# Performance work log

Hardware: AMD Instinct MI355X
Metric: run time of the kernel (lower is better)

The kernel has to match this reference:

```python
import jax, jax.numpy as jnp
import numpy as np

B, E, FC_N = 8, 65536, 2500
CONVS = [5, 16, 32, 64, 64]
EPS = 1e-5


def setup_inputs() -> dict:
    key = jax.random.key(0)
    ks = iter(jax.random.split(key, 32))
    inp = {
        'x': jax.random.normal(next(ks), (B, 5, E), dtype=jnp.float32),
        'gemm': jax.random.randint(next(ks), (B, E, 4), 0, E, dtype=jnp.int32),
        'old_verts': jax.random.normal(next(ks), (B, 642, 3), dtype=jnp.float32),
    }
    for i in range(4):
        ci, co = CONVS[i], CONVS[i + 1]
        inp[f'w{i}'] = jax.random.normal(next(ks), (co, ci, 5), dtype=jnp.float32) * 0.02
        inp[f'b{i}'] = jnp.zeros((co,), dtype=jnp.float32)
        inp[f'g{i}'] = jnp.ones((co,), dtype=jnp.float32)
        inp[f'beta{i}'] = jnp.zeros((co,), dtype=jnp.float32)
    inp['dw1'] = jax.random.normal(next(ks), (FC_N, CONVS[-1]), dtype=jnp.float32) * 0.02
    inp['db1'] = jnp.zeros((FC_N,), dtype=jnp.float32)
    inp['dw2'] = jax.random.normal(next(ks), (642 * 3, FC_N), dtype=jnp.float32) * 0.02
    inp['db2'] = jnp.zeros((642 * 3,), dtype=jnp.float32)
    return inp


def mesh_conv(x, gemm, w, b):
    # x: (B,C,E); gemm: (B,E,4) -> neighbor features (B,C,E,4)
    nb = jax.vmap(lambda xb, gb: xb[:, gb])(x, gemm)
    # MeshCNN symmetric features: [self, a+c, b+d, |a-c|, |b-d|]
    f = jnp.stack([
        x,
        nb[..., 0] + nb[..., 2],
        nb[..., 1] + nb[..., 3],
        jnp.abs(nb[..., 0] - nb[..., 2]),
        jnp.abs(nb[..., 1] - nb[..., 3]),
    ], axis=-1)  # (B,C,E,5)
    return jnp.einsum('bcek,ock->boe', f, w) + b[None, :, None]


def bn_relu(x, g, beta):
    # BatchNorm2d training-mode math over (batch, spatial) per channel
    mean = jnp.mean(x, axis=(0, 2), keepdims=True)
    var = jnp.var(x, axis=(0, 2), keepdims=True)
    return jax.nn.relu((x - mean) * jax.lax.rsqrt(var + EPS) * g[None, :, None] + beta[None, :, None])


def reference(x, gemm, old_verts,
              w0, b0, g0, beta0, w1, b1, g1, beta1,
              w2, b2, g2, beta2, w3, b3, g3, beta3,
              dw1, db1, dw2, db2):
    h = x[:, :5]
    params = [(w0, b0, g0, beta0), (w1, b1, g1, beta1),
              (w2, b2, g2, beta2), (w3, b3, g3, beta3)]
    for w, b, g, beta in params:
        h = bn_relu(mesh_conv(h, gemm, w, b), g, beta)
    pooled = jnp.mean(h, axis=2)                 # AvgPool1d(n_edges) -> (B, C)
    h1 = jax.nn.relu(pooled @ dw1.T + db1)       # dropout = identity (eval)
    out = h1 @ dw2.T + db2
    return out.reshape(-1, 642, 3) + old_verts
```

## Files before the change

kernel.cpp:

```cpp
#include <hip/hip_runtime.h>

#define E_DIM 65536
#define BE_TOTAL 524288
#define EPS_BN 1e-5f
#define NB_STATS 256

typedef unsigned int uint;
typedef unsigned short ushort;
typedef unsigned char uchar;
typedef __attribute__((ext_vector_type(4))) float floatx4;

#define PB_FP8 ((size_t)BE_TOTAL*16)

__device__ __forceinline__ float bflo(uint u){ return __uint_as_float(u << 16); }
__device__ __forceinline__ float bfhi(uint u){ return __uint_as_float(u & 0xffff0000u); }

__device__ __forceinline__ ushort pbf1(float a){
  uint ua = __float_as_uint(a);
  return (ushort)((ua + 0x7fffu + ((ua >> 16) & 1u)) >> 16);
}
__device__ __forceinline__ uint packbf(float a, float b){
  return (uint)pbf1(a) | ((uint)pbf1(b) << 16);
}
__device__ __forceinline__ void unpack8(uint4 v, float* x){
  x[0]=bflo(v.x); x[1]=bfhi(v.x); x[2]=bflo(v.y); x[3]=bfhi(v.y);
  x[4]=bflo(v.z); x[5]=bfhi(v.z); x[6]=bflo(v.w); x[7]=bfhi(v.w);
}

__device__ __forceinline__ uint2 pack8f8(const float* z){
  int lo = __builtin_amdgcn_cvt_pk_fp8_f32(z[0], z[1], 0,  false);
  lo     = __builtin_amdgcn_cvt_pk_fp8_f32(z[2], z[3], lo, true);
  int hi = __builtin_amdgcn_cvt_pk_fp8_f32(z[4], z[5], 0,  false);
  hi     = __builtin_amdgcn_cvt_pk_fp8_f32(z[6], z[7], hi, true);
  uint2 r; r.x = (uint)lo; r.y = (uint)hi; return r;
}
__device__ __forceinline__ void dec8f8(uint2 w, float* x){
  x[0]=__builtin_amdgcn_cvt_f32_fp8((int)w.x,0);
  x[1]=__builtin_amdgcn_cvt_f32_fp8((int)w.x,1);
  x[2]=__builtin_amdgcn_cvt_f32_fp8((int)w.x,2);
  x[3]=__builtin_amdgcn_cvt_f32_fp8((int)w.x,3);
  x[4]=__builtin_amdgcn_cvt_f32_fp8((int)w.y,0);
  x[5]=__builtin_amdgcn_cvt_f32_fp8((int)w.y,1);
  x[6]=__builtin_amdgcn_cvt_f32_fp8((int)w.y,2);
  x[7]=__builtin_amdgcn_cvt_f32_fp8((int)w.y,3);
}
__device__ __forceinline__ uchar f8byte(float v){
  return (uchar)(__builtin_amdgcn_cvt_pk_fp8_f32(v, 0.f, 0, false) & 0xff);
}

template<int CI, int CO>
__global__ void wprep8(const float* __restrict__ w, uchar* __restrict__ img)
{
  constexpr int CHUNKS = CI/16;
  const int t = blockIdx.x*256 + threadIdx.x;
  if (t >= CHUNKS*3*CO*4) return;
  const int g  = t & 3;
  const int o  = (t >> 2) % CO;
  const int ck = (t >> 2) / CO;
  const int chunk = ck / 3;
  const int ks    = ck % 3;
  float z[8];
  #pragma unroll
  for (int j8=0;j8<8;j8++){
    const int j = g*8 + j8;
    const int ft = ks*2 + (j>>4);
    const int ci = chunk*16 + (j & 15);
    z[j8] = (ft < 5) ? w[((size_t)o*CI + ci)*5 + ft] * 64.f : 0.f;
  }
  const int t4 = (o&3) ^ ((o>>2)&3);
  *reinterpret_cast<uint2*>(img + ((size_t)(ck*CO + o))*32 + ((g^t4)<<3)) = pack8f8(z);
}

template<int CI, int CO>
__launch_bounds__(512, 1)
__global__ void mconv_mfma(const char* __restrict__ hin,
                           const int* __restrict__ gemm,
                           const char* __restrict__ wimg,
                           const float* __restrict__ bias, float bscale,
                           const float* __restrict__ ss, float pkf,
                           char* __restrict__ hout,
                           float* __restrict__ spart)
{
  constexpr int CHUNKS = CI/16;
  constexpr int NT = CO/16;
  constexpr int FBY = 3*256*32;
  constexpr int NBUF = (CHUNKS > 1) ? 2 : 1;
  constexpr int OBB = 256*CO;
  constexpr int SBY = 8*2*CO*4;
  constexpr int SMEM = (NBUF*FBY > OBB+SBY) ? NBUF*FBY : (OBB+SBY);
  __shared__ char smem[SMEM];
  char* FB = smem;

  const int tid = threadIdx.x;
  const int bid = blockIdx.x;
  const int b   = bid & 7;
  const int e0  = (bid >> 3) * 256;
  const size_t bbase = (size_t)b << 16;

  const int lane = tid & 63;
  const int wv   = tid >> 6;
  const int col  = lane & 15;
  const int kg   = lane >> 4;
  const int t4c  = (col & 3) ^ ((col >> 2) & 3);

  floatx4 acc[2][NT];
  #pragma unroll
  for (int n=0;n<NT;n++){
    const float bv = bias[n*16 + col] * bscale;
    #pragma unroll
    for (int mt=0;mt<2;mt++) acc[mt][n] = (floatx4){bv,bv,bv,bv};
  }

  const int el = tid >> 1;
  const int hh = tid & 1;
  const int t4e = (el&3) ^ ((el>>2)&3);
  uint off[5];
  {
    const size_t idx = bbase + (size_t)(e0 + el);
    const int4 g4 = *reinterpret_cast<const int4*>(gemm + idx*4);
    off[0] = (uint)(idx*16 + hh*8);
    off[1] = (uint)((bbase + (size_t)(uint)g4.x)*16 + hh*8);
    off[2] = (uint)((bbase + (size_t)(uint)g4.y)*16 + hh*8);
    off[3] = (uint)((bbase + (size_t)(uint)g4.z)*16 + hh*8);
    off[4] = (uint)((bbase + (size_t)(uint)g4.w)*16 + hh*8);
  }

  auto BUILD = [&](uint2 (&q)[5], int chunk, char* FBb){
    float v[5][8];
    #pragma unroll
    for (int r=0;r<5;r++) dec8f8(q[r], v[r]);
    const int cb = chunk*16 + hh*8;
    #pragma unroll
    for (int c=0;c<8;c++){
      const float sc = ss[cb+c], sh = ss[CI+cb+c];
      #pragma unroll
      for (int r=0;r<5;r++) v[r][c] = fmaxf(fmaf(v[r][c], sc, sh), 0.f);
    }
    float y[5][8];
    #pragma unroll
    for (int c=0;c<8;c++){
      y[0][c] = v[0][c];
      y[1][c] = v[1][c] + v[3][c];
      y[2][c] = v[2][c] + v[4][c];
      y[3][c] = fabsf(v[1][c] - v[3][c]);
      y[4][c] = fabsf(v[2][c] - v[4][c]);
    }
    #pragma unroll
    for (int ks=0; ks<3; ks++){
      char* base = FBb + ks*8192 + el*32;
      *reinterpret_cast<uint2*>(base + (((0+hh)^t4e)<<3)) = pack8f8(y[2*ks]);
      if (ks < 2){
        *reinterpret_cast<uint2*>(base + (((2+hh)^t4e)<<3)) = pack8f8(y[2*ks+1]);
      } else {
        uint2 zz; zz.x=0u; zz.y=0u;
        *reinterpret_cast<uint2*>(base + (((2+hh)^t4e)<<3)) = zz;
      }
    }
  };

  auto MMA = [&](int chunk, const char* FBb){
    const char* WG = wimg + (size_t)chunk*(3*CO*32);
    #pragma unroll
    for (int ks=0; ks<3; ks++){
      long long bf[NT];
      #pragma unroll
      for (int n=0;n<NT;n++)
        bf[n] = *reinterpret_cast<const long long*>(WG + ks*(CO*32) + n*512 + col*32 + ((kg^t4c)<<3));
      #pragma unroll
      for (int mt=0;mt<2;mt++){
        const long long af = *reinterpret_cast<const long long*>(
            FBb + ks*8192 + (wv*32+mt*16+col)*32 + ((kg^t4c)<<3));
        #pragma unroll
        for (int n=0;n<NT;n++)
          acc[mt][n] = __builtin_amdgcn_mfma_f32_16x16x32_fp8_fp8(af, bf[n], acc[mt][n], 0, 0, 0);
      }
    }
  };

  if constexpr (CHUNKS == 1){
    uint2 q[5];
    #pragma unroll
    for (int r=0;r<5;r++) q[r] = *reinterpret_cast<const uint2*>(hin + off[r]);
    BUILD(q, 0, FB);
    __syncthreads();
    MMA(0, FB);
  } else {
    uint2 qs[2][5];
    #pragma unroll
    for (int r=0;r<5;r++) qs[0][r] = *reinterpret_cast<const uint2*>(hin + off[r]);
    {
      const char* hp1 = hin + PB_FP8;
      #pragma unroll
      for (int r=0;r<5;r++) qs[1][r] = *reinterpret_cast<const uint2*>(hp1 + off[r]);
    }
    BUILD(qs[0], 0, FB);
    __syncthreads();
    #pragma unroll
    for (int c=0; c<CHUNKS; ++c){
      if (c+2 < CHUNKS){
        const char* hp = hin + (size_t)(c+2)*PB_FP8;
        #pragma unroll
        for (int r=0;r<5;r++) qs[c&1][r] = *reinterpret_cast<const uint2*>(hp + off[r]);
      }
      MMA(c, FB + (c&1)*FBY);
      if (c+1 < CHUNKS){
        BUILD(qs[(c+1)&1], c+1, FB + ((c+1)&1)*FBY);
        __syncthreads();
      }
    }
  }

  float sred[2*NT];
  #pragma unroll
  for (int n=0;n<NT;n++){
    float s = 0.f, q2 = 0.f;
    #pragma unroll
    for (int mt=0;mt<2;mt++){
      #pragma unroll
      for (int r=0;r<4;r++){ const float vv = acc[mt][n][r]; s += vv; q2 = fmaf(vv,vv,q2); }
    }
    s  += __shfl_xor(s,16,64);  s  += __shfl_xor(s,32,64);
    q2 += __shfl_xor(q2,16,64); q2 += __shfl_xor(q2,32,64);
    sred[n] = s; sred[NT+n] = q2;
  }

  __syncthreads();
  float* SB = reinterpret_cast<float*>(smem + OBB);
  {
    uchar* OB = reinterpret_cast<uchar*>(smem);
    #pragma unroll
    for (int mt=0; mt<2; mt++){
      const int er = wv*32 + mt*16 + 4*kg;
      #pragma unroll
      for (int n=0;n<NT;n++){
        #pragma unroll
        for (int r=0;r<4;r++)
          OB[(er+r)*CO + n*16 + col] = f8byte(acc[mt][n][r] * pkf);
      }
    }
  }
  if (kg == 0){
    #pragma unroll
    for (int n=0;n<NT;n++){
      SB[wv*2*CO + n*16 + col]      = sred[n];
      SB[wv*2*CO + CO + n*16 + col] = sred[NT+n];
    }
  }
  __syncthreads();
  {
    constexpr int NV = 256*CO/16;
    for (int i=tid; i<NV; i+=512){
      const int pl  = i >> 8;
      const int elx = i & 255;
      const uint4 vv = *reinterpret_cast<const uint4*>(smem + elx*CO + pl*16);
      *reinterpret_cast<uint4*>(hout + (size_t)pl*PB_FP8 + (bbase + (size_t)(e0+elx))*16) = vv;
    }
  }
  if (tid < 2*CO){
    float s = 0.f;
    #pragma unroll
    for (int w8=0; w8<8; w8++) s += SB[w8*2*CO + tid];
    spart[(size_t)bid*2*CO + tid] = s;
  }
}

__launch_bounds__(256)
__global__ void conv0_kernel(const ushort* __restrict__ hin,
                             const int* __restrict__ gemm,
                             const float* __restrict__ w,
                             const float* __restrict__ bias,
                             char* __restrict__ hout)
{
  const int bid = blockIdx.x;
  const int swz = (bid & 7) * 256 + (bid >> 3);
  const int idx = swz * 256 + threadIdx.x;
  const int b = idx >> 16;
  const int4 g4 = *reinterpret_cast<const int4*>(gemm + (size_t)idx * 4);
  const size_t bbase = (size_t)b << 16;
  float xc[8], n0[8], n1[8], n2[8], n3[8];
  unpack8(*reinterpret_cast<const uint4*>(hin + (size_t)idx*8), xc);
  unpack8(*reinterpret_cast<const uint4*>(hin + (bbase + (size_t)(uint)g4.x)*8), n0);
  unpack8(*reinterpret_cast<const uint4*>(hin + (bbase + (size_t)(uint)g4.y)*8), n1);
  unpack8(*reinterpret_cast<const uint4*>(hin + (bbase + (size_t)(uint)g4.z)*8), n2);
  unpack8(*reinterpret_cast<const uint4*>(hin + (bbase + (size_t)(uint)g4.w)*8), n3);
  float f1[5], f2[5], f3[5], f4[5];
  #pragma unroll
  for (int c=0;c<5;c++){
    f1[c] = n0[c] + n2[c];
    f2[c] = n1[c] + n3[c];
    f3[c] = fabsf(n0[c] - n2[c]);
    f4[c] = fabsf(n1[c] - n3[c]);
  }
  float acc[16];
  #pragma unroll
  for (int o=0;o<16;o++){
    const float* wp = w + (size_t)o*25;
    float a = bias[o];
    #pragma unroll
    for (int c=0;c<5;c++){
      a = fmaf(xc[c], wp[c*5+0], a);
      a = fmaf(f1[c], wp[c*5+1], a);
      a = fmaf(f2[c], wp[c*5+2], a);
      a = fmaf(f3[c], wp[c*5+3], a);
      a = fmaf(f4[c], wp[c*5+4], a);
    }
    acc[o] = a * 16.f;
  }
  const uint2 lo = pack8f8(acc);
  const uint2 hi = pack8f8(acc + 8);
  uint4 v; v.x = lo.x; v.y = lo.y; v.z = hi.x; v.w = hi.y;
  *reinterpret_cast<uint4*>(hout + (size_t)idx * 16) = v;
}

__launch_bounds__(256)
__global__ void stats8_16(const char* __restrict__ h, float* __restrict__ part)
{
  const int tid = threadIdx.x;
  const int cg  = tid & 1;
  const int row = tid >> 1;
  float s[8], q[8];
  #pragma unroll
  for (int i=0;i<8;i++){ s[i]=0.f; q[i]=0.f; }
  for (long idx = (long)blockIdx.x*128 + row; idx < BE_TOTAL; idx += (long)gridDim.x*128){
    uint2 v = *reinterpret_cast<const uint2*>(h + idx*16 + cg*8);
    float x[8]; dec8f8(v, x);
    #pragma unroll
    for (int i=0;i<8;i++){ s[i]+=x[i]; q[i]+=x[i]*x[i]; }
  }
  __shared__ float lds[256*16];
  #pragma unroll
  for (int i=0;i<8;i++){ lds[tid*16+i]=s[i]; lds[tid*16+8+i]=q[i]; }
  __syncthreads();
  if (tid < 32){
    const int st = tid / 16;
    const int c  = tid % 16;
    const int cgg = c >> 3, ci = c & 7;
    float t = 0.f;
    for (int r=0;r<128;r++) t += lds[(r*2+cgg)*16 + st*8 + ci];
    part[(size_t)blockIdx.x*32 + tid] = t;
  }
}

template<int CO>
__launch_bounds__(256)
__global__ void merge_stats(const float* __restrict__ in, float* __restrict__ out)
{
  const int t = threadIdx.x;
  if (t >= 2*CO) return;
  const int j = blockIdx.x;
  float s = 0.f;
  #pragma unroll 4
  for (int r = 0; r < 32; r++) s += in[((size_t)(j*32 + r))*(2*CO) + t];
  out[(size_t)j*(2*CO) + t] = s;
}

template<int CO>
__launch_bounds__(256)
__global__ void finalize_stats(const float* __restrict__ part, int nblk,
                               const float* __restrict__ g, const float* __restrict__ beta,
                               float invSa, float invSt, float* __restrict__ ss)
{
  constexpr int Q = 256 / CO;
  const int t = threadIdx.x;
  const int c = t % CO;
  const int qq = t / CO;
  float s = 0.f, sq = 0.f;
  for (int b = qq; b < nblk; b += Q){
    s  += part[(size_t)b*2*CO + c];
    sq += part[(size_t)b*2*CO + CO + c];
  }
  __shared__ float lsum[256], lsq[256];
  lsum[t] = s; lsq[t] = sq;
  __syncthreads();
  if (t < CO){
    float ts = 0.f, tq = 0.f;
    #pragma unroll
    for (int r = 0; r < Q; r++){ ts += lsum[r*CO + t]; tq += lsq[r*CO + t]; }
    const float inv = 1.f / (float)BE_TOTAL;
    const float mean = ts * inv * invSa;
    const float var  = tq * inv * invSa * invSa - mean*mean;
    const float scale = g[t] * rsqrtf(var + EPS_BN);
    ss[t]      = scale * invSt;
    ss[CO + t] = beta[t] - mean * scale;
  }
}

__launch_bounds__(256)
__global__ void pool_kernel(const char* __restrict__ h3, const float* __restrict__ ss,
                            float* __restrict__ part)
{
  const int tid = threadIdx.x;
  const int cg  = tid % 8;
  const int row = tid / 8;
  const int b   = blockIdx.x >> 6;
  const int blk = blockIdx.x & 63;
  float sc[8], sh[8];
  #pragma unroll
  for (int i=0;i<8;i++){ sc[i]=ss[cg*8+i]; sh[i]=ss[64+cg*8+i]; }
  float s[8];
  #pragma unroll
  for (int i=0;i<8;i++) s[i]=0.f;
  const char* hp = h3 + (size_t)(cg>>1)*PB_FP8 + (cg&1)*8;
  for (int e = blk*32 + row; e < E_DIM; e += 64*32){
    size_t idx = ((size_t)b << 16) + e;
    uint2 v = *reinterpret_cast<const uint2*>(hp + idx*16);
    float x[8]; dec8f8(v, x);
    #pragma unroll
    for (int i=0;i<8;i++) s[i] += fmaxf(fmaf(x[i], sc[i], sh[i]), 0.f);
  }
  __shared__ float lds[256*8];
  #pragma unroll
  for (int i=0;i<8;i++) lds[tid*8+i]=s[i];
  __syncthreads();
  if (tid < 64){
    const int c = tid, cgg = c >> 3, ci = c & 7;
    float t = 0.f;
    for (int r=0;r<32;r++) t += lds[(r*8+cgg)*8 + ci];
    part[((size_t)b*64 + blk)*64 + c] = t;
  }
}

__global__ void finalize_pool(const float* __restrict__ part, float* __restrict__ pooled)
{
  const int t = threadIdx.x;
  const int b = t >> 6, c = t & 63;
  float s = 0.f;
  for (int blk=0;blk<64;blk++) s += part[((size_t)b*64 + blk)*64 + c];
  pooled[t] = s * (1.f / (float)E_DIM);
}

__global__ void fc1_kernel(const float* __restrict__ pooled, const float* __restrict__ dw1,
                           const float* __restrict__ db1, float* __restrict__ h1t)
{
  const int n = blockIdx.x*blockDim.x + threadIdx.x;
  if (n >= 2500) return;
  float acc[8];
  const float bias = db1[n];
  #pragma unroll
  for (int b=0;b<8;b++) acc[b]=bias;
  const float* wr = dw1 + (size_t)n*64;
  #pragma unroll
  for (int c=0;c<64;c++){
    float wv = wr[c];
    #pragma unroll
    for (int b=0;b<8;b++) acc[b] = fmaf(wv, pooled[b*64+c], acc[b]);
  }
  #pragma unroll
  for (int b=0;b<8;b++) h1t[(size_t)n*8 + b] = fmaxf(acc[b], 0.f);
}

__launch_bounds__(256)
__global__ void fc2_kernel(const float* __restrict__ h1t, const float* __restrict__ dw2,
                           const float* __restrict__ db2, const float* __restrict__ oldv,
                           float* __restrict__ out)
{
  const int wv   = threadIdx.x >> 6;
  const int lane = threadIdx.x & 63;
  const int m = blockIdx.x*4 + wv;
  if (m >= 1926) return;
  const float4* wr = reinterpret_cast<const float4*>(dw2 + (size_t)m*2500);
  float acc[8];
  #pragma unroll
  for (int b=0;b<8;b++) acc[b]=0.f;
  for (int j = lane; j < 625; j += 64){
    const float4 w4 = wr[j];
    const float4* hp = reinterpret_cast<const float4*>(h1t + (size_t)j*32);
    const float4 h0a = hp[0], h0b = hp[1];
    const float4 h1a = hp[2], h1b = hp[3];
    const float4 h2a = hp[4], h2b = hp[5];
    const float4 h3a = hp[6], h3b = hp[7];
    acc[0] = fmaf(w4.x, h0a.x, fmaf(w4.y, h1a.x, fmaf(w4.z, h2a.x, fmaf(w4.w, h3a.x, acc[0]))));
    acc[1] = fmaf(w4.x, h0a.y, fmaf(w4.y, h1a.y, fmaf(w4.z, h2a.y, fmaf(w4.w, h3a.y, acc[1]))));
    acc[2] = fmaf(w4.x, h0a.z, fmaf(w4.y, h1a.z, fmaf(w4.z, h2a.z, fmaf(w4.w, h3a.z, acc[2]))));
    acc[3] = fmaf(w4.x, h0a.w, fmaf(w4.y, h1a.w, fmaf(w4.z, h2a.w, fmaf(w4.w, h3a.w, acc[3]))));
    acc[4] = fmaf(w4.x, h0b.x, fmaf(w4.y, h1b.x, fmaf(w4.z, h2b.x, fmaf(w4.w, h3b.x, acc[4]))));
    acc[5] = fmaf(w4.x, h0b.y, fmaf(w4.y, h1b.y, fmaf(w4.z, h2b.y, fmaf(w4.w, h3b.y, acc[5]))));
    acc[6] = fmaf(w4.x, h0b.z, fmaf(w4.y, h1b.z, fmaf(w4.z, h2b.z, fmaf(w4.w, h3b.z, acc[6]))));
    acc[7] = fmaf(w4.x, h0b.w, fmaf(w4.y, h1b.w, fmaf(w4.z, h2b.w, fmaf(w4.w, h3b.w, acc[7]))));
  }
  #pragma unroll
  for (int s=1; s<64; s<<=1){
    #pragma unroll
    for (int b=0;b<8;b++) acc[b] += __shfl_xor(acc[b], s, 64);
  }
  if (lane == 0){
    const float bm = db2[m];
    #pragma unroll
    for (int b=0;b<8;b++){
      const int t = b*1926 + m;
      out[t] = acc[b] + bm + oldv[t];
    }
  }
}

__launch_bounds__(256)
__global__ void transpose_x(const float* __restrict__ x, ushort* __restrict__ xt)
{
  const int idx = blockIdx.x*256 + threadIdx.x;
  const int b = idx >> 16, e = idx & 65535;
  const float* xb = x + (size_t)b*5*E_DIM + e;
  uint4 v;
  v.x = packbf(xb[0],               xb[(size_t)E_DIM]);
  v.y = packbf(xb[2*(size_t)E_DIM], xb[3*(size_t)E_DIM]);
  v.z = packbf(xb[4*(size_t)E_DIM], 0.f);
  v.w = 0u;
  *reinterpret_cast<uint4*>(xt + (size_t)idx*8) = v;
}

extern "C" void kernel_launch(void* const* d_in, const int* in_sizes, int n_in,
                              void* d_out, int out_size, void* d_ws, size_t ws_size,
                              hipStream_t stream)
{
  const float* x    = (const float*)d_in[0];
  const int*   gm   = (const int*)d_in[1];
  const float* oldv = (const float*)d_in[2];
  const float* w0 = (const float*)d_in[3],  *b0 = (const float*)d_in[4];
  const float* g0 = (const float*)d_in[5],  *be0= (const float*)d_in[6];
  const float* w1 = (const float*)d_in[7],  *b1 = (const float*)d_in[8];
  const float* g1 = (const float*)d_in[9],  *be1= (const float*)d_in[10];
  const float* w2 = (const float*)d_in[11], *b2 = (const float*)d_in[12];
  const float* g2 = (const float*)d_in[13], *be2= (const float*)d_in[14];
  const float* w3 = (const float*)d_in[15], *b3 = (const float*)d_in[16];
  const float* g3 = (const float*)d_in[17], *be3= (const float*)d_in[18];
  const float* dw1 = (const float*)d_in[19], *db1 = (const float*)d_in[20];
  const float* dw2 = (const float*)d_in[21], *db2 = (const float*)d_in[22];

  char* ws = (char*)d_ws;
  size_t off = 0;
  auto alloc = [&](size_t n){ size_t o = off; off += (n + 255) & ~(size_t)255; return o; };
  ushort* xt = (ushort*)(ws + alloc((size_t)BE_TOTAL*8*2));
  char*   h0 = (char*)  (ws + alloc((size_t)BE_TOTAL*16));
  char*   h1 = (char*)  (ws + alloc((size_t)BE_TOTAL*32));
  char*   h2 = (char*)  (ws + alloc((size_t)BE_TOTAL*64));
  char*   h3 = (char*)  (ws + alloc((size_t)BE_TOTAL*64));
  float* part   = (float*)(ws + alloc((size_t)NB_STATS*128*4));
  float* spart  = (float*)(ws + alloc((size_t)2048*128*4));
  float* mpart  = (float*)(ws + alloc((size_t)64*128*4));
  float* ss0    = (float*)(ws + alloc(512));
  float* ss1    = (float*)(ws + alloc(512));
  float* ss2    = (float*)(ws + alloc(512));
  float* ss3    = (float*)(ws + alloc(512));
  float* ppart  = (float*)(ws + alloc((size_t)8*64*64*4));
  float* pooled = (float*)(ws + alloc(512*4));
  float* h1fc   = (float*)(ws + alloc(20000*4));
  uchar*  w1i   = (uchar*) (ws + alloc((size_t)3*32*32));
  uchar*  w2i   = (uchar*) (ws + alloc((size_t)6*64*32));
  uchar*  w3i   = (uchar*) (ws + alloc((size_t)12*64*32));
  (void)ws_size; (void)in_sizes; (void)n_in; (void)out_size;

  const int CB  = BE_TOTAL/256;
  const int MB2 = BE_TOTAL/256;

  transpose_x<<<CB,256,0,stream>>>(x, xt);
  wprep8<16,32><<<2,256,0,stream>>>(w1, w1i);
  wprep8<32,64><<<6,256,0,stream>>>(w2, w2i);
  wprep8<64,64><<<12,256,0,stream>>>(w3, w3i);

  conv0_kernel<<<CB,256,0,stream>>>(xt, gm, w0, b0, h0);
  stats8_16<<<NB_STATS,256,0,stream>>>(h0, part);
  finalize_stats<16><<<1,256,0,stream>>>(part, NB_STATS, g0, be0, 1.f/16.f, 1.f/16.f, ss0);

  mconv_mfma<16,32><<<MB2,512,0,stream>>>(
      h0, gm, (const char*)w1i, b1, 64.f, ss0, 0.25f, h1, spart);
  merge_stats<32><<<64,256,0,stream>>>(spart, mpart);
  finalize_stats<32><<<1,256,0,stream>>>(mpart, 64, g1, be1, 1.f/64.f, 1.f/16.f, ss1);

  mconv_mfma<32,64><<<MB2,512,0,stream>>>(
      h1, gm, (const char*)w2i, b2, 64.f, ss1, 0.25f, h2, spart);
  merge_stats<64><<<64,256,0,stream>>>(spart, mpart);
  finalize_stats<64><<<1,256,0,stream>>>(mpart, 64, g2, be2, 1.f/64.f, 1.f/16.f, ss2);

  mconv_mfma<64,64><<<MB2,512,0,stream>>>(
      h2, gm, (const char*)w3i, b3, 64.f, ss2, 0.25f, h3, spart);
  merge_stats<64><<<64,256,0,stream>>>(spart, mpart);
  finalize_stats<64><<<1,256,0,stream>>>(mpart, 64, g3, be3, 1.f/64.f, 1.f/16.f, ss3);

  pool_kernel<<<512,256,0,stream>>>(h3, ss3, ppart);
  finalize_pool<<<1,512,0,stream>>>(ppart, pooled);
  fc1_kernel<<<10,256,0,stream>>>(pooled, dw1, db1, h1fc);
  fc2_kernel<<<482,256,0,stream>>>(h1fc, dw2, db2, oldv, (float*)d_out);
}
```

Measured before the change: 248.3 us.

## Halve mconv block tile and fuse conv0 BN statistics into conv0 kernel

The MFMA mesh-conv kernel now uses 256-thread blocks over 128 edges with launch bounds requesting four blocks per CU, which shrinks the LDS footprint and doubles the grid so more blocks can stay resident. Separately, conv0 now computes per-channel sum and sum-of-squares in registers with wavefront shuffles and writes per-block partials. This removes the separate stats8_16 pass that re-read h0. Stats merging is adjusted to the larger number of partials, which adds more reduction work and lets the register budget per thread tighten.

```diff
diff --git a/kernel.cpp b/kernel.cpp
--- a/kernel.cpp
+++ b/kernel.cpp
@@ -72,7 +72,7 @@
 }
 
 template<int CI, int CO>
-__launch_bounds__(512, 1)
+__launch_bounds__(256, 4)
 __global__ void mconv_mfma(const char* __restrict__ hin,
                            const int* __restrict__ gemm,
                            const char* __restrict__ wimg,
@@ -83,10 +83,10 @@
 {
   constexpr int CHUNKS = CI/16;
   constexpr int NT = CO/16;
-  constexpr int FBY = 3*256*32;
+  constexpr int FBY = 3*128*32;
   constexpr int NBUF = (CHUNKS > 1) ? 2 : 1;
-  constexpr int OBB = 256*CO;
-  constexpr int SBY = 8*2*CO*4;
+  constexpr int OBB = 128*CO;
+  constexpr int SBY = 4*2*CO*4;
   constexpr int SMEM = (NBUF*FBY > OBB+SBY) ? NBUF*FBY : (OBB+SBY);
   __shared__ char smem[SMEM];
   char* FB = smem;
@@ -94,7 +94,7 @@
   const int tid = threadIdx.x;
   const int bid = blockIdx.x;
   const int b   = bid & 7;
-  const int e0  = (bid >> 3) * 256;
+  const int e0  = (bid >> 3) * 128;
   const size_t bbase = (size_t)b << 16;
 
   const int lane = tid & 63;
@@ -147,7 +147,7 @@
     }
     #pragma unroll
     for (int ks=0; ks<3; ks++){
-      char* base = FBb + ks*8192 + el*32;
+      char* base = FBb + ks*4096 + el*32;
       *reinterpret_cast<uint2*>(base + (((0+hh)^t4e)<<3)) = pack8f8(y[2*ks]);
       if (ks < 2){
         *reinterpret_cast<uint2*>(base + (((2+hh)^t4e)<<3)) = pack8f8(y[2*ks+1]);
@@ -169,7 +169,7 @@
       #pragma unroll
       for (int mt=0;mt<2;mt++){
         const long long af = *reinterpret_cast<const long long*>(
-            FBb + ks*8192 + (wv*32+mt*16+col)*32 + ((kg^t4c)<<3));
+            FBb + ks*4096 + (wv*32+mt*16+col)*32 + ((kg^t4c)<<3));
         #pragma unroll
         for (int n=0;n<NT;n++)
           acc[mt][n] = __builtin_amdgcn_mfma_f32_16x16x32_fp8_fp8(af, bf[n], acc[mt][n], 0, 0, 0);
@@ -248,19 +248,17 @@
   }
   __syncthreads();
   {
-    constexpr int NV = 256*CO/16;
-    for (int i=tid; i<NV; i+=512){
-      const int pl  = i >> 8;
-      const int elx = i & 255;
+    constexpr int NV = 128*CO/16;
+    for (int i=tid; i<NV; i+=256){
+      const int pl  = i >> 7;
+      const int elx = i & 127;
       const uint4 vv = *reinterpret_cast<const uint4*>(smem + elx*CO + pl*16);
       *reinterpret_cast<uint4*>(hout + (size_t)pl*PB_FP8 + (bbase + (size_t)(e0+elx))*16) = vv;
     }
   }
   if (tid < 2*CO){
-    float s = 0.f;
-    #pragma unroll
-    for (int w8=0; w8<8; w8++) s += SB[w8*2*CO + tid];
-    spart[(size_t)bid*2*CO + tid] = s;
+    spart[(size_t)bid*2*CO + tid] =
+      SB[tid] + SB[2*CO + tid] + SB[4*CO + tid] + SB[6*CO + tid];
   }
 }
 
@@ -269,7 +267,8 @@
                              const int* __restrict__ gemm,
                              const float* __restrict__ w,
                              const float* __restrict__ bias,
-                             char* __restrict__ hout)
+                             char* __restrict__ hout,
+                             float* __restrict__ spart)
 {
   const int bid = blockIdx.x;
   const int swz = (bid & 7) * 256 + (bid >> 3);
@@ -310,34 +309,29 @@
   const uint2 hi = pack8f8(acc + 8);
   uint4 v; v.x = lo.x; v.y = lo.y; v.z = hi.x; v.w = hi.y;
   *reinterpret_cast<uint4*>(hout + (size_t)idx * 16) = v;
-}
-
-__launch_bounds__(256)
-__global__ void stats8_16(const char* __restrict__ h, float* __restrict__ part)
-{
-  const int tid = threadIdx.x;
-  const int cg  = tid & 1;
-  const int row = tid >> 1;
-  float s[8], q[8];
-  #pragma unroll
-  for (int i=0;i<8;i++){ s[i]=0.f; q[i]=0.f; }
-  for (long idx = (long)blockIdx.x*128 + row; idx < BE_TOTAL; idx += (long)gridDim.x*128){
-    uint2 v = *reinterpret_cast<const uint2*>(h + idx*16 + cg*8);
-    float x[8]; dec8f8(v, x);
-    #pragma unroll
-    for (int i=0;i<8;i++){ s[i]+=x[i]; q[i]+=x[i]*x[i]; }
-  }
-  __shared__ float lds[256*16];
-  #pragma unroll
-  for (int i=0;i<8;i++){ lds[tid*16+i]=s[i]; lds[tid*16+8+i]=q[i]; }
+
+  float s[16], q[16];
+  #pragma unroll
+  for (int c=0;c<16;c++){ s[c] = acc[c]; q[c] = acc[c]*acc[c]; }
+  #pragma unroll
+  for (int d=1; d<64; d<<=1){
+    #pragma unroll
+    for (int c=0;c<16;c++){
+      s[c] += __shfl_xor(s[c], d, 64);
+      q[c] += __shfl_xor(q[c], d, 64);
+    }
+  }
+  __shared__ float sb[4*32];
+  const int wv   = threadIdx.x >> 6;
+  const int lane = threadIdx.x & 63;
+  if (lane == 0){
+    #pragma unroll
+    for (int c=0;c<16;c++){ sb[wv*32 + c] = s[c]; sb[wv*32 + 16 + c] = q[c]; }
+  }
   __syncthreads();
-  if (tid < 32){
-    const int st = tid / 16;
-    const int c  = tid % 16;
-    const int cgg = c >> 3, ci = c & 7;
-    float t = 0.f;
-    for (int r=0;r<128;r++) t += lds[(r*2+cgg)*16 + st*8 + ci];
-    part[(size_t)blockIdx.x*32 + tid] = t;
+  if (threadIdx.x < 32){
+    spart[(size_t)bid*32 + threadIdx.x] =
+      sb[threadIdx.x] + sb[32 + threadIdx.x] + sb[64 + threadIdx.x] + sb[96 + threadIdx.x];
   }
 }
 
@@ -533,9 +527,8 @@
   char*   h1 = (char*)  (ws + alloc((size_t)BE_TOTAL*32));
   char*   h2 = (char*)  (ws + alloc((size_t)BE_TOTAL*64));
   char*   h3 = (char*)  (ws + alloc((size_t)BE_TOTAL*64));
-  float* part   = (float*)(ws + alloc((size_t)NB_STATS*128*4));
-  float* spart  = (float*)(ws + alloc((size_t)2048*128*4));
-  float* mpart  = (float*)(ws + alloc((size_t)64*128*4));
+  float* spart  = (float*)(ws + alloc((size_t)4096*128*4));
+  float* mpart  = (float*)(ws + alloc((size_t)128*128*4));
   float* ss0    = (float*)(ws + alloc(512));
   float* ss1    = (float*)(ws + alloc(512));
   float* ss2    = (float*)(ws + alloc(512));
@@ -548,32 +541,32 @@
   uchar*  w3i   = (uchar*) (ws + alloc((size_t)12*64*32));
   (void)ws_size; (void)in_sizes; (void)n_in; (void)out_size;
 
-  const int CB  = BE_TOTAL/256;
-  const int MB2 = BE_TOTAL/256;
+  const int CB = BE_TOTAL/256;
+  const int MB = BE_TOTAL/128;
 
   transpose_x<<<CB,256,0,stream>>>(x, xt);
   wprep8<16,32><<<2,256,0,stream>>>(w1, w1i);
   wprep8<32,64><<<6,256,0,stream>>>(w2, w2i);
   wprep8<64,64><<<12,256,0,stream>>>(w3, w3i);
 
-  conv0_kernel<<<CB,256,0,stream>>>(xt, gm, w0, b0, h0);
-  stats8_16<<<NB_STATS,256,0,stream>>>(h0, part);
-  finalize_stats<16><<<1,256,0,stream>>>(part, NB_STATS, g0, be0, 1.f/16.f, 1.f/16.f, ss0);
-
-  mconv_mfma<16,32><<<MB2,512,0,stream>>>(
+  conv0_kernel<<<CB,256,0,stream>>>(xt, gm, w0, b0, h0, spart);
+  merge_stats<16><<<64,256,0,stream>>>(spart, mpart);
+  finalize_stats<16><<<1,256,0,stream>>>(mpart, 64, g0, be0, 1.f/16.f, 1.f/16.f, ss0);
+
+  mconv_mfma<16,32><<<MB,256,0,stream>>>(
       h0, gm, (const char*)w1i, b1, 64.f, ss0, 0.25f, h1, spart);
-  merge_stats<32><<<64,256,0,stream>>>(spart, mpart);
-  finalize_stats<32><<<1,256,0,stream>>>(mpart, 64, g1, be1, 1.f/64.f, 1.f/16.f, ss1);
-
-  mconv_mfma<32,64><<<MB2,512,0,stream>>>(
+  merge_stats<32><<<128,256,0,stream>>>(spart, mpart);
+  finalize_stats<32><<<1,256,0,stream>>>(mpart, 128, g1, be1, 1.f/64.f, 1.f/16.f, ss1);
+
+  mconv_mfma<32,64><<<MB,256,0,stream>>>(
       h1, gm, (const char*)w2i, b2, 64.f, ss1, 0.25f, h2, spart);
-  merge_stats<64><<<64,256,0,stream>>>(spart, mpart);
-  finalize_stats<64><<<1,256,0,stream>>>(mpart, 64, g2, be2, 1.f/64.f, 1.f/16.f, ss2);
-
-  mconv_mfma<64,64><<<MB2,512,0,stream>>>(
+  merge_stats<64><<<128,256,0,stream>>>(spart, mpart);
+  finalize_stats<64><<<1,256,0,stream>>>(mpart, 128, g2, be2, 1.f/64.f, 1.f/16.f, ss2);
+
+  mconv_mfma<64,64><<<MB,256,0,stream>>>(
       h2, gm, (const char*)w3i, b3, 64.f, ss2, 0.25f, h3, spart);
-  merge_stats<64><<<64,256,0,stream>>>(spart, mpart);
-  finalize_stats<64><<<1,256,0,stream>>>(mpart, 64, g3, be3, 1.f/64.f, 1.f/16.f, ss3);
+  merge_stats<64><<<128,256,0,stream>>>(spart, mpart);
+  finalize_stats<64><<<1,256,0,stream>>>(mpart, 128, g3, be3, 1.f/64.f, 1.f/16.f, ss3);
 
   pool_kernel<<<512,256,0,stream>>>(h3, ss3, ppart);
   finalize_pool<<<1,512,0,stream>>>(ppart, pooled);
```

Result: no change. 249.2 us (+0.4%).
